# Optimization experiments

Hardware: AMD Instinct MI355X
Metric: run time of the kernel (lower is better)

## Reference

```python
import jax, jax.numpy as jnp
import numpy as np
from jax import lax

N = 4096      # nodes
D = 256       # in_channels
H = 128       # hidden_size (cell output = 2*H = 256)
BLOCK = 128   # row-block size for the masked-max scan
THR = 0.99    # adjacency threshold on uniform A -> avg degree ~41
EPS = 1e-12


def _block_max(m, scores):
    # m: [BLOCK, N] bool, scores: [N, H] -> [BLOCK, H]
    v = jnp.where(m[:, :, None], scores[None, :, :], -jnp.inf)
    return v.max(axis=1)

_block_max = jax.checkpoint(_block_max)


def masked_max(mask, scores):
    # maxpool over neighbors, blocked over destination nodes to avoid an [N,N,H] temp
    n = mask.shape[0]
    mblk = mask.reshape(n // BLOCK, BLOCK, n)
    def body(_, m):
        return None, _block_max(m, scores)
    _, out = lax.scan(body, None, mblk)
    out = out.reshape(n, scores.shape[-1])
    # nodes with no neighbors -> 0
    return jnp.where(jnp.isneginf(out), jnp.zeros_like(out), out)


def setup_inputs() -> dict:
    key = jax.random.key(0)
    ks = jax.random.split(key, 16)
    def w(k, shape):
        fan = shape[0]
        return (jax.random.normal(k, shape, jnp.float32) / np.sqrt(fan)).astype(jnp.float32)
    D1 = 2 * H  # layer-1 input dim (= 256)
    return dict(
        x=jax.random.normal(ks[0], (N, D), jnp.float32),
        A=jax.random.uniform(ks[1], (N, N), dtype=jnp.float32),
        # layer 0 cell params
        Wp0=w(ks[2], (D, H)), bp0=jnp.zeros((H,), jnp.float32),
        Ws0=w(ks[3], (D, H)), bs0=jnp.zeros((H,), jnp.float32),
        Wn0=w(ks[4], (H, H)), bn0=jnp.zeros((H,), jnp.float32),
        # layer 1 cell params
        Wp1=w(ks[5], (D1, H)), bp1=jnp.zeros((H,), jnp.float32),
        Ws1=w(ks[6], (D1, H)), bs1=jnp.zeros((H,), jnp.float32),
        Wn1=w(ks[7], (H, H)), bn1=jnp.zeros((H,), jnp.float32),
    )


def _cell(x, mask, Wp, bp, Ws, bs, Wn, bn):
    # GraphSAGE maxpool cell: concat(self transform, neighbor maxpool transform)
    scores = jax.nn.relu(x @ Wp + bp)                 # [N, H]
    pooled = masked_max(mask, scores)                 # [N, H]
    return jnp.concatenate([x @ Ws + bs, pooled @ Wn + bn], axis=-1)  # [N, 2H]


def reference(x, A, Wp0, bp0, Ws0, bs0, Wn0, bn0, Wp1, bp1, Ws1, bs1, Wn1, bn1):
    mask = A > THR  # [N, N] bool adjacency
    for (Wp, bp, Ws, bs, Wn, bn) in ((Wp0, bp0, Ws0, bs0, Wn0, bn0),
                                     (Wp1, bp1, Ws1, bs1, Wn1, bn1)):
        x = _cell(x, mask, Wp, bp, Ws, bs, Wn, bn)
        x = jax.nn.relu(x)
        nrm = jnp.linalg.norm(x, axis=-1, keepdims=True)
        x = x / jnp.maximum(nrm, EPS)
    return x
```

## Files before the change

kernel.cpp:

```cpp
#include <hip/hip_runtime.h>

#define NN 4096
#define CAP 256
#define THRV 0.99f

typedef __attribute__((ext_vector_type(8))) short short8v;
typedef __attribute__((ext_vector_type(4))) float f32x4;

__device__ inline unsigned short f2bf(float f) {
  unsigned u = __builtin_bit_cast(unsigned, f);
  u = (u + 0x7fffu + ((u >> 16) & 1u)) >> 16;
  return (unsigned short)u;
}
__device__ inline unsigned pkmax(unsigned a, unsigned b) {
  unsigned r;
  asm("v_pk_max_u16 %0, %1, %2" : "=v"(r) : "v"(a), "v"(b));
  return r;
}
__device__ inline uint4 max4(uint4 a, uint4 b) {
  return make_uint4(pkmax(a.x, b.x), pkmax(a.y, b.y), pkmax(a.z, b.z), pkmax(a.w, b.w));
}


__global__ __launch_bounds__(256) void k_gp(
    const float* __restrict__ x,
    const float* __restrict__ Wp0, const float* __restrict__ bp0,
    const float* __restrict__ Ws0, const float* __restrict__ bs0,
    const float* __restrict__ Wn0, const float* __restrict__ Wp1,
    const float* __restrict__ Ws1, const float* __restrict__ Wn1,
    unsigned short* __restrict__ scores0, float* __restrict__ S0,
    unsigned short* __restrict__ tWn0, unsigned short* __restrict__ tWp1,
    unsigned short* __restrict__ tWs1, unsigned short* __restrict__ tWn1) {
  __shared__ unsigned short smw[32768];
  const int bid = blockIdx.x;
  const int tid = threadIdx.x;

  if (bid < 128) {
    const int set = bid >> 6;
    const float* W = set ? Ws0 : Wp0;
    const float* bias = set ? bs0 : bp0;
#pragma unroll
    for (int it = 0; it < 32; ++it) {
      int e0 = it * 1024 + tid * 4;
      float4 v = *(const float4*)(W + e0);
      int k = e0 >> 7, n = e0 & 127;
      int elem = (k & 3) + 4 * ((k >> 4) & 1);
      int gg = (k >> 2) & 3;
      int kt8 = (k >> 5) * 8;
      float vv[4] = {v.x, v.y, v.z, v.w};
#pragma unroll
      for (int i = 0; i < 4; ++i) {
        int nn = n + i;
        smw[((kt8 + (nn >> 4)) << 9) + ((gg * 16 + (nn & 15)) << 3) + elem] = f2bf(vv[i]);
      }
    }
    __syncthreads();
    const int wv = tid >> 6, lane = tid & 63;
    const int g = lane >> 4, r15 = lane & 15;
    const int rb16 = (bid & 63) * 64 + wv * 16;
    const int row = rb16 + r15;
    f32x4 acc[8] = {};
#pragma unroll
    for (int ktIdx = 0; ktIdx < 8; ++ktIdx) {
      const float* xp = x + (size_t)row * 256 + ktIdx * 32 + 4 * g;
      float4 lo = *(const float4*)xp;
      float4 hi = *(const float4*)(xp + 16);
      short8v a;
      a[0] = (short)f2bf(lo.x); a[1] = (short)f2bf(lo.y);
      a[2] = (short)f2bf(lo.z); a[3] = (short)f2bf(lo.w);
      a[4] = (short)f2bf(hi.x); a[5] = (short)f2bf(hi.y);
      a[6] = (short)f2bf(hi.z); a[7] = (short)f2bf(hi.w);
#pragma unroll
      for (int nf = 0; nf < 8; ++nf) {
        uint4 bw = *(const uint4*)(smw + ((ktIdx * 8 + nf) << 9) + lane * 8);
        acc[nf] = __builtin_amdgcn_mfma_f32_16x16x32_bf16(a, __builtin_bit_cast(short8v, bw), acc[nf], 0, 0, 0);
      }
    }
#pragma unroll
    for (int nf = 0; nf < 8; ++nf) {
      int col = nf * 16 + r15;
      float bv = bias[col];
#pragma unroll
      for (int r = 0; r < 4; ++r) {
        int orow = rb16 + 4 * g + r;
        float t = acc[nf][r] + bv;
        if (set == 0) scores0[(size_t)orow * 128 + col] = f2bf(fmaxf(t, 0.f));
        else          S0[(size_t)orow * 128 + col] = t;
      }
    }
    return;
  }
  int id = bid - 128;
  const float* src; unsigned short* dst; int base;
  if (id < 16)      { src = Wn0; dst = tWn0; base = id; }
  else if (id < 48) { src = Wp1; dst = tWp1; base = id - 16; }
  else if (id < 80) { src = Ws1; dst = tWs1; base = id - 48; }
  else              { src = Wn1; dst = tWn1; base = id - 80; }
  int e0 = base * 1024 + tid * 4;
  float4 v = *(const float4*)(src + e0);
  int k = e0 >> 7, n = e0 & 127;
  float vv[4] = {v.x, v.y, v.z, v.w};
  int elem = (k & 3) + 4 * ((k >> 4) & 1);
  int gg = (k >> 2) & 3;
  int fragkt = (k >> 5) * 8;
#pragma unroll
  for (int i = 0; i < 4; ++i) {
    int nn = n + i;
    int idx = ((fragkt + (nn >> 4)) << 9) + ((gg * 16 + (nn & 15)) << 3) + elem;
    dst[idx] = f2bf(vv[i]);
  }
}

template<int LAYER>
__global__ __launch_bounds__(512) void fusedL(
    const float* __restrict__ A,
    int* __restrict__ cnt, unsigned short* __restrict__ nbr,
    const unsigned short* __restrict__ scores_in, const float* __restrict__ S_in,
    const unsigned short* __restrict__ tWn, const float* __restrict__ bn,
    const unsigned short* __restrict__ tWp, const float* __restrict__ bp,
    const unsigned short* __restrict__ tWs, const float* __restrict__ bs,
    unsigned short* __restrict__ scores_out, float* __restrict__ S_out,
    float* __restrict__ out) {
  __shared__ int scnt[16];
  __shared__ unsigned short snb[16][CAP];
  __shared__ unsigned short pool2[16][2][136];
  __shared__ unsigned short pooled[16][136];
  __shared__ unsigned short xb[16][264];
  __shared__ float ssqs[16];
  __shared__ float ssqw[4][16];

  const int tid = threadIdx.x;
  const int wv = tid >> 6, lane = tid & 63, g = lane >> 4, r15 = lane & 15;
  const int r0 = blockIdx.x * 16;

  if (LAYER == 0) {
    if (tid < 16) scnt[tid] = 0;
    __syncthreads();
    const float4* Ar = (const float4*)(A + (size_t)r0 * NN);
    float4 c0 = Ar[tid], c1 = Ar[tid + 512];
    for (int r = 0; r < 16; ++r) {
      float4 n0 = c0, n1 = c1;
      if (r < 15) {
        const float4* nx = Ar + (size_t)(r + 1) * (NN / 4);
        n0 = nx[tid]; n1 = nx[tid + 512];
      }
      unsigned m = 0;
      m |= (c0.x > THRV) ? 0x1u : 0u;  m |= (c0.y > THRV) ? 0x2u : 0u;
      m |= (c0.z > THRV) ? 0x4u : 0u;  m |= (c0.w > THRV) ? 0x8u : 0u;
      m |= (c1.x > THRV) ? 0x10u : 0u; m |= (c1.y > THRV) ? 0x20u : 0u;
      m |= (c1.z > THRV) ? 0x40u : 0u; m |= (c1.w > THRV) ? 0x80u : 0u;
      int cntT = __popc(m);
      int inc = cntT;
#pragma unroll
      for (int off = 1; off < 64; off <<= 1) {
        int o = __shfl_up(inc, off, 64);
        if (lane >= off) inc += o;
      }
      int excl = inc - cntT;
      int wtot = __shfl(inc, 63, 64);
      int wbase = 0;
      if (lane == 0) wbase = atomicAdd(&scnt[r], wtot);
      wbase = __shfl(wbase, 0, 64);
      int pos = wbase + excl;
      while (m) {
        int b = __ffs(m) - 1;
        m &= m - 1;
        if (pos < CAP) snb[r][pos] = (unsigned short)(4 * tid + 2048 * (b >> 2) + (b & 3));
        ++pos;
      }
      c0 = n0; c1 = n1;
    }
    __syncthreads();
    if (tid < 16) { int c = min(scnt[tid], CAP); scnt[tid] = c; cnt[r0 + tid] = c; }
    __syncthreads();
    {
      ushort4* dst = (ushort4*)(nbr + (size_t)r0 * CAP);
      const ushort4* s = (const ushort4*)snb;
      dst[tid] = s[tid];
      dst[tid + 512] = s[tid + 512];
    }
  } else {
    if (tid < 16) scnt[tid] = cnt[r0 + tid];
    {
      const ushort4* src = (const ushort4*)(nbr + (size_t)r0 * CAP);
      ushort4* dst = (ushort4*)snb;
      dst[tid] = src[tid];
      dst[tid + 512] = src[tid + 512];
    }
    __syncthreads();
  }

  {
    const int r = tid >> 5, sub = tid & 31;
    const int h = sub >> 4, c8 = (sub & 15) * 8;
    const int c = scnt[r];
    uint4 m0 = make_uint4(0, 0, 0, 0), m1 = m0, m2 = m0, m3 = m0;
    int k = h;
    for (; k + 6 < c; k += 8) {
      int j0 = snb[r][k], j1 = snb[r][k + 2], j2 = snb[r][k + 4], j3 = snb[r][k + 6];
      uint4 a0 = *(const uint4*)(scores_in + (size_t)j0 * 128 + c8);
      uint4 a1 = *(const uint4*)(scores_in + (size_t)j1 * 128 + c8);
      uint4 a2 = *(const uint4*)(scores_in + (size_t)j2 * 128 + c8);
      uint4 a3 = *(const uint4*)(scores_in + (size_t)j3 * 128 + c8);
      m0 = max4(m0, a0); m1 = max4(m1, a1); m2 = max4(m2, a2); m3 = max4(m3, a3);
    }
    for (; k < c; k += 2)
      m0 = max4(m0, *(const uint4*)(scores_in + (size_t)snb[r][k] * 128 + c8));
    *(uint4*)&pool2[r][h][c8] = max4(max4(m0, m1), max4(m2, m3));
  }
  __syncthreads();
  if (tid < 256) {
    const int r = tid >> 4, c8 = (tid & 15) * 8;
    uint4 a = *(const uint4*)&pool2[r][0][c8];
    uint4 b = *(const uint4*)&pool2[r][1][c8];
    *(uint4*)&pooled[r][c8] = max4(a, b);
  }
  __syncthreads();

  float sv[8];
  f32x4 pacc[2] = {};
  const int srow = tid >> 4, sc8 = (tid & 15) * 8;
  if (tid < 256) {
    const float* sp = S_in + (size_t)(r0 + srow) * 128 + sc8;
    float4 sa = *(const float4*)sp;
    float4 sb = *(const float4*)(sp + 4);
    sv[0] = fmaxf(sa.x, 0.f); sv[1] = fmaxf(sa.y, 0.f);
    sv[2] = fmaxf(sa.z, 0.f); sv[3] = fmaxf(sa.w, 0.f);
    sv[4] = fmaxf(sb.x, 0.f); sv[5] = fmaxf(sb.y, 0.f);
    sv[6] = fmaxf(sb.z, 0.f); sv[7] = fmaxf(sb.w, 0.f);
    float ps = 0.f;
#pragma unroll
    for (int i = 0; i < 8; ++i) ps += sv[i] * sv[i];
#pragma unroll
    for (int off = 1; off < 16; off <<= 1) ps += __shfl_xor(ps, off, 16);
    if ((tid & 15) == 0) ssqs[srow] = ps;
  } else {
    const int wv2 = wv - 4;
#pragma unroll
    for (int kt = 0; kt < 128; kt += 32) {
      ushort4 alo = *(const ushort4*)&pooled[r15][kt + 4 * g];
      ushort4 ahi = *(const ushort4*)&pooled[r15][kt + 16 + 4 * g];
      short8v a;
      a[0] = alo.x; a[1] = alo.y; a[2] = alo.z; a[3] = alo.w;
      a[4] = ahi.x; a[5] = ahi.y; a[6] = ahi.z; a[7] = ahi.w;
#pragma unroll
      for (int f = 0; f < 2; ++f) {
        uint4 bw = *((const uint4*)(tWn + (size_t)((kt >> 5) * 8 + 2 * wv2 + f) * 512) + lane);
        pacc[f] = __builtin_amdgcn_mfma_f32_16x16x32_bf16(a, __builtin_bit_cast(short8v, bw), pacc[f], 0, 0, 0);
      }
    }
#pragma unroll
    for (int f = 0; f < 2; ++f) {
      float bv = bn[(2 * wv2 + f) * 16 + r15];
#pragma unroll
      for (int rr = 0; rr < 4; ++rr) pacc[f][rr] = fmaxf(pacc[f][rr] + bv, 0.f);
    }
#pragma unroll
    for (int rr = 0; rr < 4; ++rr) {
      float ps = pacc[0][rr] * pacc[0][rr] + pacc[1][rr] * pacc[1][rr];
#pragma unroll
      for (int off = 1; off < 16; off <<= 1) ps += __shfl_xor(ps, off, 16);
      if (r15 == 0) ssqw[wv2][4 * g + rr] = ps;
    }
  }
  __syncthreads();

  if (LAYER == 0) {
    if (tid < 256) {
      float tot = ssqs[srow] + ssqw[0][srow] + ssqw[1][srow] + ssqw[2][srow] + ssqw[3][srow];
      float sc = 1.f / fmaxf(sqrtf(tot), 1e-12f);
      unsigned short hh[8];
#pragma unroll
      for (int i = 0; i < 8; ++i) hh[i] = f2bf(sv[i] * sc);
      uint4 wvv;
      wvv.x = (unsigned)hh[0] | ((unsigned)hh[1] << 16);
      wvv.y = (unsigned)hh[2] | ((unsigned)hh[3] << 16);
      wvv.z = (unsigned)hh[4] | ((unsigned)hh[5] << 16);
      wvv.w = (unsigned)hh[6] | ((unsigned)hh[7] << 16);
      *(uint4*)&xb[srow][sc8] = wvv;
    } else {
      const int wv2 = wv - 4;
#pragma unroll
      for (int rr = 0; rr < 4; ++rr) {
        int row = 4 * g + rr;
        float tot = ssqs[row] + ssqw[0][row] + ssqw[1][row] + ssqw[2][row] + ssqw[3][row];
        float sc = 1.f / fmaxf(sqrtf(tot), 1e-12f);
#pragma unroll
        for (int f = 0; f < 2; ++f)
          xb[row][128 + (2 * wv2 + f) * 16 + r15] = f2bf(pacc[f][rr] * sc);
      }
    }
    __syncthreads();
    const int s = wv >> 2;
    const unsigned short* Wt = s ? tWs : tWp;
    const float* bb = s ? bs : bp;
    const int nf0 = (wv & 3) * 2;
    f32x4 dacc[2] = {};
#pragma unroll
    for (int kt = 0; kt < 256; kt += 32) {
      ushort4 alo = *(const ushort4*)&xb[r15][kt + 4 * g];
      ushort4 ahi = *(const ushort4*)&xb[r15][kt + 16 + 4 * g];
      short8v a;
      a[0] = alo.x; a[1] = alo.y; a[2] = alo.z; a[3] = alo.w;
      a[4] = ahi.x; a[5] = ahi.y; a[6] = ahi.z; a[7] = ahi.w;
#pragma unroll
      for (int f = 0; f < 2; ++f) {
        uint4 bw = *((const uint4*)(Wt + (size_t)((kt >> 5) * 8 + nf0 + f) * 512) + lane);
        dacc[f] = __builtin_amdgcn_mfma_f32_16x16x32_bf16(a, __builtin_bit_cast(short8v, bw), dacc[f], 0, 0, 0);
      }
    }
#pragma unroll
    for (int f = 0; f < 2; ++f) {
      int col = (nf0 + f) * 16 + r15;
      float bv = bb[col];
#pragma unroll
      for (int rr = 0; rr < 4; ++rr) {
        int grow = r0 + 4 * g + rr;
        float t = dacc[f][rr] + bv;
        if (s == 0) scores_out[(size_t)grow * 128 + col] = f2bf(fmaxf(t, 0.f));
        else        S_out[(size_t)grow * 128 + col] = t;
      }
    }
  } else {
    if (tid < 256) {
      float tot = ssqs[srow] + ssqw[0][srow] + ssqw[1][srow] + ssqw[2][srow] + ssqw[3][srow];
      float sc = 1.f / fmaxf(sqrtf(tot), 1e-12f);
      float* op = out + (size_t)(r0 + srow) * 256 + sc8;
      *(float4*)op = make_float4(sv[0] * sc, sv[1] * sc, sv[2] * sc, sv[3] * sc);
      *(float4*)(op + 4) = make_float4(sv[4] * sc, sv[5] * sc, sv[6] * sc, sv[7] * sc);
    } else {
      const int wv2 = wv - 4;
#pragma unroll
      for (int rr = 0; rr < 4; ++rr) {
        int row = 4 * g + rr;
        float tot = ssqs[row] + ssqw[0][row] + ssqw[1][row] + ssqw[2][row] + ssqw[3][row];
        float sc = 1.f / fmaxf(sqrtf(tot), 1e-12f);
#pragma unroll
        for (int f = 0; f < 2; ++f)
          out[(size_t)(r0 + row) * 256 + 128 + (2 * wv2 + f) * 16 + r15] = pacc[f][rr] * sc;
      }
    }
  }
}

extern "C" void kernel_launch(void* const* d_in, const int* in_sizes, int n_in,
                              void* d_out, int out_size, void* d_ws, size_t ws_size,
                              hipStream_t stream) {
  (void)in_sizes; (void)n_in; (void)out_size; (void)ws_size;
  const float* x   = (const float*)d_in[0];
  const float* A   = (const float*)d_in[1];
  const float* Wp0 = (const float*)d_in[2];
  const float* bp0 = (const float*)d_in[3];
  const float* Ws0 = (const float*)d_in[4];
  const float* bs0 = (const float*)d_in[5];
  const float* Wn0 = (const float*)d_in[6];
  const float* bn0 = (const float*)d_in[7];
  const float* Wp1 = (const float*)d_in[8];
  const float* bp1 = (const float*)d_in[9];
  const float* Ws1 = (const float*)d_in[10];
  const float* bs1 = (const float*)d_in[11];
  const float* Wn1 = (const float*)d_in[12];
  const float* bn1 = (const float*)d_in[13];

  char* ws = (char*)d_ws;
  auto alloc = [&](size_t bytes) { char* p = ws; ws += (bytes + 255) & ~(size_t)255; return p; };
  int* cnt             = (int*)alloc((size_t)NN * 4);
  unsigned short* nbr  = (unsigned short*)alloc((size_t)NN * CAP * 2);
  unsigned short* tWn0 = (unsigned short*)alloc(128 * 128 * 2);
  unsigned short* tWp1 = (unsigned short*)alloc(256 * 128 * 2);
  unsigned short* tWs1 = (unsigned short*)alloc(256 * 128 * 2);
  unsigned short* tWn1 = (unsigned short*)alloc(128 * 128 * 2);
  unsigned short* scores0 = (unsigned short*)alloc((size_t)NN * 128 * 2);
  unsigned short* scores1 = (unsigned short*)alloc((size_t)NN * 128 * 2);
  float* S0            = (float*)alloc((size_t)NN * 128 * 4);
  float* S1            = (float*)alloc((size_t)NN * 128 * 4);

  k_gp<<<224, 256, 0, stream>>>(x, Wp0, bp0, Ws0, bs0, Wn0, Wp1, Ws1, Wn1,
                                scores0, S0, tWn0, tWp1, tWs1, tWn1);
  fusedL<0><<<NN / 16, 512, 0, stream>>>(A, cnt, nbr, scores0, S0,
                                         tWn0, bn0, tWp1, bp1, tWs1, bs1,
                                         scores1, S1, nullptr);
  fusedL<1><<<NN / 16, 512, 0, stream>>>(A, cnt, nbr, scores1, S1,
                                         tWn1, bn1, nullptr, nullptr, nullptr, nullptr,
                                         nullptr, nullptr, (float*)d_out);
}
```

Measured before the change: 50.02 us.

## Precompute adjacency bitmask in separate kernel; rebuild neighbor lists per layer

A new kernel scans the dense A matrix once and writes a packed 64-bit bitmask per row (2 MB instead of reading 64 MB later). Both fused layers now rebuild neighbor lists in shared memory from the bitmask using per-element shared atomics, which removes the serial per-row A scan with wave prefix sums from layer 0 and the global cnt/nbr lists. The trade-off is an extra kernel launch, a serial dependency before the layer kernels, and a neighbor order that is no longer deterministic. Because the maximum is order-independent, the results are unaffected.

```diff
diff --git a/kernel.cpp b/kernel.cpp
--- a/kernel.cpp
+++ b/kernel.cpp
@@ -6,6 +6,7 @@
 
 typedef __attribute__((ext_vector_type(8))) short short8v;
 typedef __attribute__((ext_vector_type(4))) float f32x4;
+typedef unsigned long long u64;
 
 __device__ inline unsigned short f2bf(float f) {
   unsigned u = __builtin_bit_cast(unsigned, f);
@@ -21,6 +22,27 @@
   return make_uint4(pkmax(a.x, b.x), pkmax(a.y, b.y), pkmax(a.z, b.z), pkmax(a.w, b.w));
 }
 
+
+__global__ __launch_bounds__(256) void k_scan_mask(
+    const float* __restrict__ A, u64* __restrict__ mask) {
+  const int wv = threadIdx.x >> 6, lane = threadIdx.x & 63;
+#pragma unroll
+  for (int rr = 0; rr < 2; ++rr) {
+    const int row = blockIdx.x * 8 + wv * 2 + rr;
+    const float4* Ar = (const float4*)(A + (size_t)row * NN);
+    u64 m = 0;
+#pragma unroll
+    for (int c = 0; c < 16; ++c) {
+      float4 v = Ar[c * 64 + lane];
+      const int b = c * 4;
+      m |= (v.x > THRV ? 1ull : 0ull) << b;
+      m |= (v.y > THRV ? 1ull : 0ull) << (b + 1);
+      m |= (v.z > THRV ? 1ull : 0ull) << (b + 2);
+      m |= (v.w > THRV ? 1ull : 0ull) << (b + 3);
+    }
+    mask[(size_t)row * 64 + lane] = m;
+  }
+}
 
 __global__ __launch_bounds__(256) void k_gp(
     const float* __restrict__ x,
@@ -113,8 +135,7 @@
 
 template<int LAYER>
 __global__ __launch_bounds__(512) void fusedL(
-    const float* __restrict__ A,
-    int* __restrict__ cnt, unsigned short* __restrict__ nbr,
+    const u64* __restrict__ mask,
     const unsigned short* __restrict__ scores_in, const float* __restrict__ S_in,
     const unsigned short* __restrict__ tWn, const float* __restrict__ bn,
     const unsigned short* __restrict__ tWp, const float* __restrict__ bp,
@@ -133,62 +154,27 @@
   const int wv = tid >> 6, lane = tid & 63, g = lane >> 4, r15 = lane & 15;
   const int r0 = blockIdx.x * 16;
 
-  if (LAYER == 0) {
-    if (tid < 16) scnt[tid] = 0;
-    __syncthreads();
-    const float4* Ar = (const float4*)(A + (size_t)r0 * NN);
-    float4 c0 = Ar[tid], c1 = Ar[tid + 512];
-    for (int r = 0; r < 16; ++r) {
-      float4 n0 = c0, n1 = c1;
-      if (r < 15) {
-        const float4* nx = Ar + (size_t)(r + 1) * (NN / 4);
-        n0 = nx[tid]; n1 = nx[tid + 512];
-      }
-      unsigned m = 0;
-      m |= (c0.x > THRV) ? 0x1u : 0u;  m |= (c0.y > THRV) ? 0x2u : 0u;
-      m |= (c0.z > THRV) ? 0x4u : 0u;  m |= (c0.w > THRV) ? 0x8u : 0u;
-      m |= (c1.x > THRV) ? 0x10u : 0u; m |= (c1.y > THRV) ? 0x20u : 0u;
-      m |= (c1.z > THRV) ? 0x40u : 0u; m |= (c1.w > THRV) ? 0x80u : 0u;
-      int cntT = __popc(m);
-      int inc = cntT;
-#pragma unroll
-      for (int off = 1; off < 64; off <<= 1) {
-        int o = __shfl_up(inc, off, 64);
-        if (lane >= off) inc += o;
-      }
-      int excl = inc - cntT;
-      int wtot = __shfl(inc, 63, 64);
-      int wbase = 0;
-      if (lane == 0) wbase = atomicAdd(&scnt[r], wtot);
-      wbase = __shfl(wbase, 0, 64);
-      int pos = wbase + excl;
+  if (tid < 16) scnt[tid] = 0;
+  __syncthreads();
+  {
+    const int r = tid >> 5, w0 = tid & 31;
+    const u64* mrow = mask + (size_t)(r0 + r) * 64;
+#pragma unroll
+    for (int h = 0; h < 2; ++h) {
+      int w = w0 + 32 * h;
+      u64 m = mrow[w];
       while (m) {
-        int b = __ffs(m) - 1;
+        int b = __ffsll(m) - 1;
         m &= m - 1;
-        if (pos < CAP) snb[r][pos] = (unsigned short)(4 * tid + 2048 * (b >> 2) + (b & 3));
-        ++pos;
-      }
-      c0 = n0; c1 = n1;
-    }
-    __syncthreads();
-    if (tid < 16) { int c = min(scnt[tid], CAP); scnt[tid] = c; cnt[r0 + tid] = c; }
-    __syncthreads();
-    {
-      ushort4* dst = (ushort4*)(nbr + (size_t)r0 * CAP);
-      const ushort4* s = (const ushort4*)snb;
-      dst[tid] = s[tid];
-      dst[tid + 512] = s[tid + 512];
-    }
-  } else {
-    if (tid < 16) scnt[tid] = cnt[r0 + tid];
-    {
-      const ushort4* src = (const ushort4*)(nbr + (size_t)r0 * CAP);
-      ushort4* dst = (ushort4*)snb;
-      dst[tid] = src[tid];
-      dst[tid + 512] = src[tid + 512];
-    }
-    __syncthreads();
-  }
+        int col = 256 * (b >> 2) + 4 * w + (b & 3);
+        int pos = atomicAdd(&scnt[r], 1);
+        if (pos < CAP) snb[r][pos] = (unsigned short)col;
+      }
+    }
+  }
+  __syncthreads();
+  if (tid < 16) scnt[tid] = min(scnt[tid], CAP);
+  __syncthreads();
 
   {
     const int r = tid >> 5, sub = tid & 31;
@@ -364,8 +350,7 @@
 
   char* ws = (char*)d_ws;
   auto alloc = [&](size_t bytes) { char* p = ws; ws += (bytes + 255) & ~(size_t)255; return p; };
-  int* cnt             = (int*)alloc((size_t)NN * 4);
-  unsigned short* nbr  = (unsigned short*)alloc((size_t)NN * CAP * 2);
+  u64* mask            = (u64*)alloc((size_t)NN * 64 * 8);
   unsigned short* tWn0 = (unsigned short*)alloc(128 * 128 * 2);
   unsigned short* tWp1 = (unsigned short*)alloc(256 * 128 * 2);
   unsigned short* tWs1 = (unsigned short*)alloc(256 * 128 * 2);
@@ -375,12 +360,13 @@
   float* S0            = (float*)alloc((size_t)NN * 128 * 4);
   float* S1            = (float*)alloc((size_t)NN * 128 * 4);
 
+  k_scan_mask<<<NN / 8, 256, 0, stream>>>(A, mask);
   k_gp<<<224, 256, 0, stream>>>(x, Wp0, bp0, Ws0, bs0, Wn0, Wp1, Ws1, Wn1,
                                 scores0, S0, tWn0, tWp1, tWs1, tWn1);
-  fusedL<0><<<NN / 16, 512, 0, stream>>>(A, cnt, nbr, scores0, S0,
+  fusedL<0><<<NN / 16, 512, 0, stream>>>(mask, scores0, S0,
                                          tWn0, bn0, tWp1, bp1, tWs1, bs1,
                                          scores1, S1, nullptr);
-  fusedL<1><<<NN / 16, 512, 0, stream>>>(A, cnt, nbr, scores1, S1,
+  fusedL<1><<<NN / 16, 512, 0, stream>>>(mask, scores1, S1,
                                          tWn1, bn1, nullptr, nullptr, nullptr, nullptr,
                                          nullptr, nullptr, (float*)d_out);
 }
```

After: 52.23 us. 4.4% more time.
